# Kernel optimization log

Hardware: AMD Instinct MI355X
Metric: run time of the kernel (lower is better)

Reference implementation:

```python
import jax, jax.numpy as jnp
import numpy as np
import math

B, T, C, H = 4, 1024, 1024, 16
D = C // H  # head dim = 64

def setup_inputs() -> dict:
    key = jax.random.key(0)
    ks = jax.random.split(key, 10)
    s = 1.0 / math.sqrt(C)
    x = jax.random.normal(ks[0], (B, T, C), dtype=jnp.float32)
    pad = (jax.random.uniform(ks[1], (B, T)) < 0.2).astype(jnp.float32)
    # ensure first token of every row is unpadded so softmax rows are well-posed
    pad = pad.at[:, 0].set(0.0)
    Wq = jax.random.normal(ks[2], (C, C), dtype=jnp.float32) * s
    bq = jnp.zeros((C,), dtype=jnp.float32)
    Wk = jax.random.normal(ks[3], (C, C), dtype=jnp.float32) * s
    bk = jnp.zeros((C,), dtype=jnp.float32)
    Wv = jax.random.normal(ks[4], (C, C), dtype=jnp.float32) * s
    bv = jnp.zeros((C,), dtype=jnp.float32)
    Wp = jax.random.normal(ks[5], (C, C), dtype=jnp.float32) * s
    bp = jnp.zeros((C,), dtype=jnp.float32)
    return {"x": x, "x_padding_judge": pad, "Wq": Wq, "bq": bq,
            "Wk": Wk, "bk": bk, "Wv": Wv, "bv": bv, "Wp": Wp, "bp": bp}

def reference(x, x_padding_judge, Wq, bq, Wk, bk, Wv, bv, Wp, bp):
    # keep flag: 1.0 where token is real, 0.0 where padded
    keep = 1.0 - x_padding_judge                      # [B, T]
    mask = keep[:, :, None] * keep[:, None, :]        # [B, T, T] outer product
    # projections, split heads: [B, H, T, D]
    def heads(w, b):
        return (x @ w + b).reshape(B, T, H, D).transpose(0, 2, 1, 3)
    q, k, v = heads(Wq, bq), heads(Wk, bk), heads(Wv, bv)
    att = jnp.einsum('bhqd,bhkd->bhqk', q, k) * (1.0 / math.sqrt(D))
    # attn_pdrop=0 => att_full is all ones; masked_fill where mask == 0
    att = jnp.where(mask[:, None, :, :] == 0, -1e9, att)
    att = jax.nn.softmax(att, axis=-1)
    y = jnp.einsum('bhqk,bhkd->bhqd', att, v)         # [B, H, T, D]
    y = y.transpose(0, 2, 1, 3).reshape(B, T, C)
    return y @ Wp + bp
```

## Files before the change

kernel.cpp:

```cpp
#include <hip/hip_runtime.h>
#include <hip/hip_bf16.h>
#include <math.h>

#define Bb 4
#define Tt 1024
#define Cc 1024
#define Hh 16
#define Dd 64

typedef __attribute__((ext_vector_type(8))) _Float16 half8;
typedef __attribute__((ext_vector_type(4))) _Float16 half4;
typedef __attribute__((ext_vector_type(4))) float floatx4;


__global__ __launch_bounds__(256) void convert_fp16(const float* __restrict__ s,
                                                    _Float16* __restrict__ d)
{
    const int m16 = blockIdx.x;
    const int r   = threadIdx.x & 15;
    const int kc0 = threadIdx.x >> 4;
    const float* src = s + (size_t)(m16 * 16 + r) * 1024;
    _Float16*   dst = d + (size_t)m16 * 16384 + r * 8;
#pragma unroll
    for (int c8 = 0; c8 < 8; ++c8) {
        const int kc = kc0 + c8 * 16;
        float4 a = *(const float4*)(src + kc * 8);
        float4 b = *(const float4*)(src + kc * 8 + 4);
        half8 h;
        h[0] = (_Float16)a.x; h[1] = (_Float16)a.y; h[2] = (_Float16)a.z; h[3] = (_Float16)a.w;
        h[4] = (_Float16)b.x; h[5] = (_Float16)b.y; h[6] = (_Float16)b.z; h[7] = (_Float16)b.w;
        *(half8*)(dst + kc * 128) = h;
    }
}

struct WPrep { const float* W[4]; _Float16* out[4]; };

__global__ __launch_bounds__(256) void prep_weights(WPrep p)
{
    const int z = blockIdx.z;
    const float* __restrict__ W = p.W[z];
    _Float16* __restrict__ outp = p.out[z];
    __shared__ float tile[64][65];
    const int k0  = blockIdx.y * 64;
    const int n0  = blockIdx.x * 64;
    const int tr  = threadIdx.x >> 4;
    const int tc4 = (threadIdx.x & 15) * 4;

#pragma unroll
    for (int i = 0; i < 4; ++i) {
        const int kk = tr + i * 16;
        float4 v = *(const float4*)(W + (size_t)(k0 + kk) * 1024 + n0 + tc4);
        tile[kk][tc4 + 0] = v.x;
        tile[kk][tc4 + 1] = v.y;
        tile[kk][tc4 + 2] = v.z;
        tile[kk][tc4 + 3] = v.w;
    }
    __syncthreads();
#pragma unroll
    for (int i = 0; i < 4; ++i) {
        half4 h;
#pragma unroll
        for (int c = 0; c < 4; ++c) h[c] = (_Float16)tile[tc4 + c][tr + i * 16];
        _Float16* dst = outp + (size_t)((n0 >> 4) + i) * 16384
                        + ((k0 + tc4) >> 3) * 128 + tr * 8 + (tc4 & 7);
        *(half4*)dst = h;
    }
}

struct QkvP { const _Float16* Wt[3]; const float* bias[3];
              _Float16* qb; _Float16* kb; _Float16* vt; };

__global__ __launch_bounds__(256) void gemm_qkv(const _Float16* __restrict__ xh, QkvP p)
{
    const int z = blockIdx.z;
    const _Float16* __restrict__ Wt   = p.Wt[z];
    const float* __restrict__    bias = p.bias[z];

    const int tid  = threadIdx.x;
    const int lane = tid & 63;
    const int w    = tid >> 6;
    const int wr   = w >> 1, wc = w & 1;
    const int quad = lane >> 4;
    const int l15  = lane & 15;
    const int bm   = blockIdx.x * 128;
    const int bn   = blockIdx.y * 128;

    const _Float16* Ap[4];
    const _Float16* Bp[4];
#pragma unroll
    for (int i = 0; i < 4; ++i)
        Ap[i] = xh + (size_t)((bm >> 4) + wr * 4 + i) * 16384 + lane * 8;
#pragma unroll
    for (int j = 0; j < 4; ++j)
        Bp[j] = Wt + (size_t)((bn >> 4) + wc * 4 + j) * 16384 + lane * 8;

    floatx4 acc[4][4];
#pragma unroll
    for (int i = 0; i < 4; ++i)
#pragma unroll
        for (int j = 0; j < 4; ++j)
            acc[i][j] = (floatx4){0.f, 0.f, 0.f, 0.f};

    half8 a0[4], b0[4];
#pragma unroll
    for (int i = 0; i < 4; ++i) a0[i] = *(const half8*)(Ap[i]);
#pragma unroll
    for (int j = 0; j < 4; ++j) b0[j] = *(const half8*)(Bp[j]);

    for (int kt = 0; kt < 1024; kt += 64) {
        half8 a1[4], b1[4];
        const size_t o1 = (size_t)(kt + 32) * 16;
#pragma unroll
        for (int i = 0; i < 4; ++i) a1[i] = *(const half8*)(Ap[i] + o1);
#pragma unroll
        for (int j = 0; j < 4; ++j) b1[j] = *(const half8*)(Bp[j] + o1);
#pragma unroll
        for (int i = 0; i < 4; ++i)
#pragma unroll
            for (int j = 0; j < 4; ++j)
                acc[i][j] = __builtin_amdgcn_mfma_f32_16x16x32_f16(a0[i], b0[j], acc[i][j], 0, 0, 0);

        const size_t o2 = (kt + 64 < 1024) ? (size_t)(kt + 64) * 16 : 0;
#pragma unroll
        for (int i = 0; i < 4; ++i) a0[i] = *(const half8*)(Ap[i] + o2);
#pragma unroll
        for (int j = 0; j < 4; ++j) b0[j] = *(const half8*)(Bp[j] + o2);
#pragma unroll
        for (int i = 0; i < 4; ++i)
#pragma unroll
            for (int j = 0; j < 4; ++j)
                acc[i][j] = __builtin_amdgcn_mfma_f32_16x16x32_f16(a1[i], b1[j], acc[i][j], 0, 0, 0);
    }

    if (z == 2) {
#pragma unroll
        for (int j = 0; j < 4; ++j) {
            const int col = bn + wc * 64 + j * 16 + l15;
            const int h  = col >> 6;
            const float bj = bias[col];
#pragma unroll
            for (int i = 0; i < 4; ++i) {
                const int t0 = bm + wr * 64 + i * 16 + quad * 4;
                const int bh = (t0 >> 10) * 16 + h;
                const int tm = t0 & 1023;
                half4 pk;
#pragma unroll
                for (int r = 0; r < 4; ++r) pk[r] = (_Float16)(acc[i][j][r] + bj);
                *(half4*)(p.vt + (size_t)bh * 65536 + (size_t)j * 16384
                          + (tm >> 3) * 128 + l15 * 8 + (tm & 7)) = pk;
            }
        }
    } else {
        _Float16* outp = (z == 0) ? p.qb : p.kb;
#pragma unroll
        for (int j = 0; j < 4; ++j) {
            const int col = bn + wc * 64 + j * 16 + l15;
            const int h  = col >> 6;
            const int dd = col & 63;
            const float bj = bias[col];
            const int doff = (dd >> 3) * 128 + (dd & 7);
#pragma unroll
            for (int i = 0; i < 4; ++i) {
#pragma unroll
                for (int r = 0; r < 4; ++r) {
                    const int tg = bm + wr * 64 + i * 16 + quad * 4 + r;
                    const int bh = (tg >> 10) * 16 + h;
                    const int tm = tg & 1023;
                    outp[(size_t)bh * 65536 + (tm >> 4) * 1024 + doff + (tm & 15) * 8] =
                        (_Float16)(acc[i][j][r] + bj);
                }
            }
        }
    }
}

__global__ __launch_bounds__(256) void attn_mfma(
    const _Float16* __restrict__ qb, const _Float16* __restrict__ kb,
    const _Float16* __restrict__ vt, const float* __restrict__ padj,
    _Float16* __restrict__ yh)
{
    __shared__ __align__(16) _Float16 Ps[4][2048];

    const int tid  = threadIdx.x;
    const int lane = tid & 63;
    const int w    = tid >> 6;
    const int quad = lane >> 4;
    const int l15  = lane & 15;
    const int bh   = blockIdx.x;
    const int q0   = blockIdx.y * 128;
    const int b    = bh >> 4;
    const int h    = bh & 15;

    const _Float16* qf = qb + (size_t)bh * 65536;
    const _Float16* kf = kb + (size_t)bh * 65536;
    const _Float16* vf = vt + (size_t)bh * 65536;
    const float*    pk_row = padj + b * Tt;

    half8 bq[2][2];
#pragma unroll
    for (int ks = 0; ks < 2; ++ks)
#pragma unroll
        for (int nq = 0; nq < 2; ++nq)
            bq[ks][nq] = *(const half8*)(qf + (size_t)((q0 >> 4) + w * 2 + nq) * 1024
                                         + ks * 512 + lane * 8);
    float kq[2];
#pragma unroll
    for (int nq = 0; nq < 2; ++nq)
        kq[nq] = 1.0f - pk_row[q0 + w * 32 + nq * 16 + l15];

    floatx4 O[2][4];
    floatx4 l_acc[2];
#pragma unroll
    for (int mi = 0; mi < 2; ++mi) {
#pragma unroll
        for (int dj = 0; dj < 4; ++dj) O[mi][dj] = (floatx4){0.f, 0.f, 0.f, 0.f};
        l_acc[mi] = (floatx4){0.f, 0.f, 0.f, 0.f};
    }
    half8 ones;
#pragma unroll
    for (int j = 0; j < 8; ++j) ones[j] = (_Float16)1.0f;

    constexpr float SC = 0.18033688011112042f;

    for (int kt = 0; kt < Tt; kt += 64) {
        half8 ak[2][4], bv[2][4];
#pragma unroll
        for (int ks = 0; ks < 2; ++ks)
#pragma unroll
            for (int mk = 0; mk < 4; ++mk)
                ak[ks][mk] = *(const half8*)(kf + (size_t)((kt >> 4) + mk) * 1024
                                             + ks * 512 + lane * 8);
#pragma unroll
        for (int ks = 0; ks < 2; ++ks)
#pragma unroll
            for (int dj = 0; dj < 4; ++dj)
                bv[ks][dj] = *(const half8*)(vf + (size_t)dj * 16384 + (kt >> 3) * 128
                                             + ks * 512 + lane * 8);
        float4 kk4[4];
#pragma unroll
        for (int mk = 0; mk < 4; ++mk)
            kk4[mk] = *(const float4*)(pk_row + kt + mk * 16 + quad * 4);

        floatx4 ST[4][2];
#pragma unroll
        for (int mk = 0; mk < 4; ++mk)
#pragma unroll
            for (int nq = 0; nq < 2; ++nq)
                ST[mk][nq] = (floatx4){0.f, 0.f, 0.f, 0.f};
#pragma unroll
        for (int ks = 0; ks < 2; ++ks)
#pragma unroll
            for (int mk = 0; mk < 4; ++mk)
#pragma unroll
                for (int nq = 0; nq < 2; ++nq)
                    ST[mk][nq] = __builtin_amdgcn_mfma_f32_16x16x32_f16(
                        ak[ks][mk], bq[ks][nq], ST[mk][nq], 0, 0, 0);

#pragma unroll
        for (int mk = 0; mk < 4; ++mk) {
            const float kkr[4] = {1.0f - kk4[mk].x, 1.0f - kk4[mk].y,
                                  1.0f - kk4[mk].z, 1.0f - kk4[mk].w};
#pragma unroll
            for (int nq = 0; nq < 2; ++nq) {
                half4 pk;
#pragma unroll
                for (int r = 0; r < 4; ++r) {
                    const float e = __builtin_amdgcn_exp2f(ST[mk][nq][r] * SC);
                    const float pv = (kq[nq] == 0.0f) ? 1.0f : kkr[r] * e;
                    pk[r] = (_Float16)pv;
                }
                *(half4*)&Ps[w][((mk * 2 + (quad >> 1)) * 32 + nq * 16 + l15) * 8
                               + (quad & 1) * 4] = pk;
            }
        }

#pragma unroll
        for (int ks = 0; ks < 2; ++ks) {
            half8 ap[2];
#pragma unroll
            for (int mi = 0; mi < 2; ++mi)
                ap[mi] = *(const half8*)&Ps[w][((ks * 4 + quad) * 32 + mi * 16 + l15) * 8];
#pragma unroll
            for (int mi = 0; mi < 2; ++mi) {
#pragma unroll
                for (int dj = 0; dj < 4; ++dj)
                    O[mi][dj] = __builtin_amdgcn_mfma_f32_16x16x32_f16(
                        ap[mi], bv[ks][dj], O[mi][dj], 0, 0, 0);
                l_acc[mi] = __builtin_amdgcn_mfma_f32_16x16x32_f16(
                    ap[mi], ones, l_acc[mi], 0, 0, 0);
            }
        }
    }

#pragma unroll
    for (int mi = 0; mi < 2; ++mi) {
#pragma unroll
        for (int r = 0; r < 4; ++r) {
            const int rowl  = w * 32 + mi * 16 + quad * 4 + r;
            const int token = b * Tt + q0 + rowl;
            const float inv = 1.0f / l_acc[mi][r];
            const size_t tb = (size_t)(token >> 4) * 16384 + (token & 15) * 8;
#pragma unroll
            for (int dj = 0; dj < 4; ++dj) {
                const int col = h * 64 + dj * 16 + l15;
                yh[tb + (col >> 3) * 128 + (col & 7)] = (_Float16)(O[mi][dj][r] * inv);
            }
        }
    }
}

__global__ __launch_bounds__(256) void gemm_proj(const _Float16* __restrict__ Ay,
                                                 const _Float16* __restrict__ Bt,
                                                 const float* __restrict__ bias,
                                                 float* __restrict__ out)
{
    const int tid  = threadIdx.x;
    const int lane = tid & 63;
    const int w    = tid >> 6;
    const int quad = lane >> 4;
    const int l15  = lane & 15;
    const int bm   = blockIdx.x * 128;
    const int bn   = blockIdx.y * 64;

    const _Float16* Ap[2];
    const _Float16* Bp[4];
#pragma unroll
    for (int i = 0; i < 2; ++i)
        Ap[i] = Ay + (size_t)((bm >> 4) + w * 2 + i) * 16384 + lane * 8;
#pragma unroll
    for (int j = 0; j < 4; ++j)
        Bp[j] = Bt + (size_t)((bn >> 4) + j) * 16384 + lane * 8;

    floatx4 acc[2][4];
#pragma unroll
    for (int i = 0; i < 2; ++i)
#pragma unroll
        for (int j = 0; j < 4; ++j)
            acc[i][j] = (floatx4){0.f, 0.f, 0.f, 0.f};

    half8 a0[2], b0[4];
#pragma unroll
    for (int i = 0; i < 2; ++i) a0[i] = *(const half8*)(Ap[i]);
#pragma unroll
    for (int j = 0; j < 4; ++j) b0[j] = *(const half8*)(Bp[j]);

    for (int kt = 0; kt < 1024; kt += 64) {
        half8 a1[2], b1[4];
        const size_t o1 = (size_t)(kt + 32) * 16;
#pragma unroll
        for (int i = 0; i < 2; ++i) a1[i] = *(const half8*)(Ap[i] + o1);
#pragma unroll
        for (int j = 0; j < 4; ++j) b1[j] = *(const half8*)(Bp[j] + o1);
#pragma unroll
        for (int i = 0; i < 2; ++i)
#pragma unroll
            for (int j = 0; j < 4; ++j)
                acc[i][j] = __builtin_amdgcn_mfma_f32_16x16x32_f16(a0[i], b0[j], acc[i][j], 0, 0, 0);

        const size_t o2 = (kt + 64 < 1024) ? (size_t)(kt + 64) * 16 : 0;
#pragma unroll
        for (int i = 0; i < 2; ++i) a0[i] = *(const half8*)(Ap[i] + o2);
#pragma unroll
        for (int j = 0; j < 4; ++j) b0[j] = *(const half8*)(Bp[j] + o2);
#pragma unroll
        for (int i = 0; i < 2; ++i)
#pragma unroll
            for (int j = 0; j < 4; ++j)
                acc[i][j] = __builtin_amdgcn_mfma_f32_16x16x32_f16(a1[i], b1[j], acc[i][j], 0, 0, 0);
    }

#pragma unroll
    for (int j = 0; j < 4; ++j) {
        const int col = bn + j * 16 + l15;
        const float bj = bias[col];
#pragma unroll
        for (int i = 0; i < 2; ++i) {
            const int row = bm + w * 32 + i * 16 + quad * 4;
            float* o = out + (size_t)row * 1024 + col;
#pragma unroll
            for (int r = 0; r < 4; ++r)
                o[(size_t)r * 1024] = acc[i][j][r] + bj;
        }
    }
}

extern "C" void kernel_launch(void* const* d_in, const int* in_sizes, int n_in,
                              void* d_out, int out_size, void* d_ws, size_t ws_size,
                              hipStream_t stream)
{
    const float* x    = (const float*)d_in[0];
    const float* padj = (const float*)d_in[1];
    const float* Wq   = (const float*)d_in[2];
    const float* bq   = (const float*)d_in[3];
    const float* Wk   = (const float*)d_in[4];
    const float* bk   = (const float*)d_in[5];
    const float* Wv   = (const float*)d_in[6];
    const float* bv   = (const float*)d_in[7];
    const float* Wp   = (const float*)d_in[8];
    const float* bp   = (const float*)d_in[9];
    float* out = (float*)d_out;

    const size_t MB = 1024 * 1024;
    char* ws = (char*)d_ws;
    _Float16* xh  = (_Float16*)(ws);
    _Float16* Wt0 = (_Float16*)(ws +  8 * MB);
    _Float16* Wt1 = (_Float16*)(ws + 10 * MB);
    _Float16* Wt2 = (_Float16*)(ws + 12 * MB);
    _Float16* Wtp = (_Float16*)(ws + 14 * MB);
    _Float16* qb  = (_Float16*)(ws + 16 * MB);
    _Float16* kb  = (_Float16*)(ws + 24 * MB);
    _Float16* vtb = (_Float16*)(ws + 32 * MB);
    _Float16* yh  = (_Float16*)(ws + 40 * MB);

    convert_fp16<<<256, 256, 0, stream>>>(x, xh);

    WPrep wp;
    wp.W[0] = Wq; wp.W[1] = Wk; wp.W[2] = Wv; wp.W[3] = Wp;
    wp.out[0] = Wt0; wp.out[1] = Wt1; wp.out[2] = Wt2; wp.out[3] = Wtp;
    prep_weights<<<dim3(16, 16, 4), 256, 0, stream>>>(wp);

    QkvP qp;
    qp.Wt[0] = Wt0; qp.Wt[1] = Wt1; qp.Wt[2] = Wt2;
    qp.bias[0] = bq; qp.bias[1] = bk; qp.bias[2] = bv;
    qp.qb = qb; qp.kb = kb; qp.vt = vtb;
    gemm_qkv<<<dim3(32, 8, 3), 256, 0, stream>>>(xh, qp);

    attn_mfma<<<dim3(64, 8), 256, 0, stream>>>(qb, kb, vtb, padj, yh);

    gemm_proj<<<dim3(32, 16), 256, 0, stream>>>(yh, Wtp, bp, out);
}
```

Baseline: 188.6 us.

## Merge prep kernels, transpose Q/K GEMM for vector stores, widen attention to 8 waves

Folds the x conversion and weight transposition into one prep_all launch to save a kernel launch. For the Q and K projections it swaps the GEMM operands (weights as A, x as B), so each lane holds four consecutive head-dim values and writes them as one half4 instead of four scalar stores. The attention kernel moves to 512 threads with 16 query rows per wave instead of 32, which halves per-wave register state and raises wave count, but each wave now gets less reuse of the K and V fragments it loads.

```diff
diff --git a/kernel.cpp b/kernel.cpp
--- a/kernel.cpp
+++ b/kernel.cpp
@@ -13,36 +13,36 @@
 typedef __attribute__((ext_vector_type(4))) float floatx4;
 
 
-__global__ __launch_bounds__(256) void convert_fp16(const float* __restrict__ s,
-                                                    _Float16* __restrict__ d)
+struct PrepP { const float* x; _Float16* xh; const float* W[4]; _Float16* out[4]; };
+
+__global__ __launch_bounds__(256) void prep_all(PrepP p)
 {
-    const int m16 = blockIdx.x;
-    const int r   = threadIdx.x & 15;
-    const int kc0 = threadIdx.x >> 4;
-    const float* src = s + (size_t)(m16 * 16 + r) * 1024;
-    _Float16*   dst = d + (size_t)m16 * 16384 + r * 8;
-#pragma unroll
-    for (int c8 = 0; c8 < 8; ++c8) {
-        const int kc = kc0 + c8 * 16;
-        float4 a = *(const float4*)(src + kc * 8);
-        float4 b = *(const float4*)(src + kc * 8 + 4);
-        half8 h;
-        h[0] = (_Float16)a.x; h[1] = (_Float16)a.y; h[2] = (_Float16)a.z; h[3] = (_Float16)a.w;
-        h[4] = (_Float16)b.x; h[5] = (_Float16)b.y; h[6] = (_Float16)b.z; h[7] = (_Float16)b.w;
-        *(half8*)(dst + kc * 128) = h;
-    }
-}
-
-struct WPrep { const float* W[4]; _Float16* out[4]; };
-
-__global__ __launch_bounds__(256) void prep_weights(WPrep p)
-{
-    const int z = blockIdx.z;
+    if (blockIdx.x < 256) {
+        const int m16 = blockIdx.x;
+        const int r   = threadIdx.x & 15;
+        const int kc0 = threadIdx.x >> 4;
+        const float* src = p.x + (size_t)(m16 * 16 + r) * 1024;
+        _Float16*   dst = p.xh + (size_t)m16 * 16384 + r * 8;
+#pragma unroll
+        for (int c8 = 0; c8 < 8; ++c8) {
+            const int kc = kc0 + c8 * 16;
+            float4 a = *(const float4*)(src + kc * 8);
+            float4 b = *(const float4*)(src + kc * 8 + 4);
+            half8 h;
+            h[0] = (_Float16)a.x; h[1] = (_Float16)a.y; h[2] = (_Float16)a.z; h[3] = (_Float16)a.w;
+            h[4] = (_Float16)b.x; h[5] = (_Float16)b.y; h[6] = (_Float16)b.z; h[7] = (_Float16)b.w;
+            *(half8*)(dst + kc * 128) = h;
+        }
+        return;
+    }
+    const int bid2 = blockIdx.x - 256;
+    const int z    = bid2 >> 8;
+    const int rem  = bid2 & 255;
+    const int n0   = (rem & 15) * 64;
+    const int k0   = (rem >> 4) * 64;
     const float* __restrict__ W = p.W[z];
     _Float16* __restrict__ outp = p.out[z];
     __shared__ float tile[64][65];
-    const int k0  = blockIdx.y * 64;
-    const int n0  = blockIdx.x * 64;
     const int tr  = threadIdx.x >> 4;
     const int tc4 = (threadIdx.x & 15) * 4;
 
@@ -73,8 +73,7 @@
 __global__ __launch_bounds__(256) void gemm_qkv(const _Float16* __restrict__ xh, QkvP p)
 {
     const int z = blockIdx.z;
-    const _Float16* __restrict__ Wt   = p.Wt[z];
-    const float* __restrict__    bias = p.bias[z];
+    const float* __restrict__ bias = p.bias[z];
 
     const int tid  = threadIdx.x;
     const int lane = tid & 63;
@@ -82,17 +81,20 @@
     const int wr   = w >> 1, wc = w & 1;
     const int quad = lane >> 4;
     const int l15  = lane & 15;
-    const int bm   = blockIdx.x * 128;
-    const int bn   = blockIdx.y * 128;
+
+    const int mb = (z == 2) ? blockIdx.x * 128 : blockIdx.y * 128;
+    const int nb = (z == 2) ? blockIdx.y * 128 : blockIdx.x * 128;
+    const _Float16* __restrict__ Abase = (z == 2) ? xh : p.Wt[z];
+    const _Float16* __restrict__ Bbase = (z == 2) ? p.Wt[2] : xh;
 
     const _Float16* Ap[4];
     const _Float16* Bp[4];
 #pragma unroll
     for (int i = 0; i < 4; ++i)
-        Ap[i] = xh + (size_t)((bm >> 4) + wr * 4 + i) * 16384 + lane * 8;
+        Ap[i] = Abase + (size_t)((mb >> 4) + wr * 4 + i) * 16384 + lane * 8;
 #pragma unroll
     for (int j = 0; j < 4; ++j)
-        Bp[j] = Wt + (size_t)((bn >> 4) + wc * 4 + j) * 16384 + lane * 8;
+        Bp[j] = Bbase + (size_t)((nb >> 4) + wc * 4 + j) * 16384 + lane * 8;
 
     floatx4 acc[4][4];
 #pragma unroll
@@ -135,12 +137,12 @@
     if (z == 2) {
 #pragma unroll
         for (int j = 0; j < 4; ++j) {
-            const int col = bn + wc * 64 + j * 16 + l15;
+            const int col = nb + wc * 64 + j * 16 + l15;
             const int h  = col >> 6;
             const float bj = bias[col];
 #pragma unroll
             for (int i = 0; i < 4; ++i) {
-                const int t0 = bm + wr * 64 + i * 16 + quad * 4;
+                const int t0 = mb + wr * 64 + i * 16 + quad * 4;
                 const int bh = (t0 >> 10) * 16 + h;
                 const int tm = t0 & 1023;
                 half4 pk;
@@ -154,32 +156,34 @@
         _Float16* outp = (z == 0) ? p.qb : p.kb;
 #pragma unroll
         for (int j = 0; j < 4; ++j) {
-            const int col = bn + wc * 64 + j * 16 + l15;
-            const int h  = col >> 6;
-            const int dd = col & 63;
-            const float bj = bias[col];
-            const int doff = (dd >> 3) * 128 + (dd & 7);
+            const int token = nb + wc * 64 + j * 16 + l15;
+            const int bi = token >> 10;
+            const int tm = token & 1023;
+            const size_t tb = (size_t)(tm >> 4) * 1024 + (tm & 15) * 8;
 #pragma unroll
             for (int i = 0; i < 4; ++i) {
-#pragma unroll
-                for (int r = 0; r < 4; ++r) {
-                    const int tg = bm + wr * 64 + i * 16 + quad * 4 + r;
-                    const int bh = (tg >> 10) * 16 + h;
-                    const int tm = tg & 1023;
-                    outp[(size_t)bh * 65536 + (tm >> 4) * 1024 + doff + (tm & 15) * 8] =
-                        (_Float16)(acc[i][j][r] + bj);
-                }
+                const int colb = mb + wr * 64 + i * 16 + quad * 4;
+                const int h  = colb >> 6;
+                const int d  = colb & 63;
+                const float4 b4 = *(const float4*)(bias + colb);
+                half4 pk;
+                pk[0] = (_Float16)(acc[i][j][0] + b4.x);
+                pk[1] = (_Float16)(acc[i][j][1] + b4.y);
+                pk[2] = (_Float16)(acc[i][j][2] + b4.z);
+                pk[3] = (_Float16)(acc[i][j][3] + b4.w);
+                *(half4*)(outp + (size_t)(bi * 16 + h) * 65536 + tb
+                          + (d >> 3) * 128 + (d & 7)) = pk;
             }
         }
     }
 }
 
-__global__ __launch_bounds__(256) void attn_mfma(
+__global__ __launch_bounds__(512) void attn_mfma(
     const _Float16* __restrict__ qb, const _Float16* __restrict__ kb,
     const _Float16* __restrict__ vt, const float* __restrict__ padj,
     _Float16* __restrict__ yh)
 {
-    __shared__ __align__(16) _Float16 Ps[4][2048];
+    __shared__ __align__(16) _Float16 Ps[8][1024];
 
     const int tid  = threadIdx.x;
     const int lane = tid & 63;
@@ -196,26 +200,17 @@
     const _Float16* vf = vt + (size_t)bh * 65536;
     const float*    pk_row = padj + b * Tt;
 
-    half8 bq[2][2];
+    half8 bq[2];
 #pragma unroll
     for (int ks = 0; ks < 2; ++ks)
-#pragma unroll
-        for (int nq = 0; nq < 2; ++nq)
-            bq[ks][nq] = *(const half8*)(qf + (size_t)((q0 >> 4) + w * 2 + nq) * 1024
-                                         + ks * 512 + lane * 8);
-    float kq[2];
-#pragma unroll
-    for (int nq = 0; nq < 2; ++nq)
-        kq[nq] = 1.0f - pk_row[q0 + w * 32 + nq * 16 + l15];
-
-    floatx4 O[2][4];
-    floatx4 l_acc[2];
-#pragma unroll
-    for (int mi = 0; mi < 2; ++mi) {
-#pragma unroll
-        for (int dj = 0; dj < 4; ++dj) O[mi][dj] = (floatx4){0.f, 0.f, 0.f, 0.f};
-        l_acc[mi] = (floatx4){0.f, 0.f, 0.f, 0.f};
-    }
+        bq[ks] = *(const half8*)(qf + (size_t)((q0 >> 4) + w) * 1024 + ks * 512 + lane * 8);
+    const float kq = 1.0f - pk_row[q0 + w * 16 + l15];
+
+    floatx4 O[4];
+    floatx4 l_acc = (floatx4){0.f, 0.f, 0.f, 0.f};
+#pragma unroll
+    for (int dj = 0; dj < 4; ++dj) O[dj] = (floatx4){0.f, 0.f, 0.f, 0.f};
+
     half8 ones;
 #pragma unroll
     for (int j = 0; j < 8; ++j) ones[j] = (_Float16)1.0f;
@@ -241,70 +236,49 @@
         for (int mk = 0; mk < 4; ++mk)
             kk4[mk] = *(const float4*)(pk_row + kt + mk * 16 + quad * 4);
 
-        floatx4 ST[4][2];
-#pragma unroll
-        for (int mk = 0; mk < 4; ++mk)
-#pragma unroll
-            for (int nq = 0; nq < 2; ++nq)
-                ST[mk][nq] = (floatx4){0.f, 0.f, 0.f, 0.f};
+        floatx4 ST[4];
+#pragma unroll
+        for (int mk = 0; mk < 4; ++mk) ST[mk] = (floatx4){0.f, 0.f, 0.f, 0.f};
 #pragma unroll
         for (int ks = 0; ks < 2; ++ks)
 #pragma unroll
             for (int mk = 0; mk < 4; ++mk)
-#pragma unroll
-                for (int nq = 0; nq < 2; ++nq)
-                    ST[mk][nq] = __builtin_amdgcn_mfma_f32_16x16x32_f16(
-                        ak[ks][mk], bq[ks][nq], ST[mk][nq], 0, 0, 0);
+                ST[mk] = __builtin_amdgcn_mfma_f32_16x16x32_f16(ak[ks][mk], bq[ks], ST[mk], 0, 0, 0);
 
 #pragma unroll
         for (int mk = 0; mk < 4; ++mk) {
             const float kkr[4] = {1.0f - kk4[mk].x, 1.0f - kk4[mk].y,
                                   1.0f - kk4[mk].z, 1.0f - kk4[mk].w};
-#pragma unroll
-            for (int nq = 0; nq < 2; ++nq) {
-                half4 pk;
-#pragma unroll
-                for (int r = 0; r < 4; ++r) {
-                    const float e = __builtin_amdgcn_exp2f(ST[mk][nq][r] * SC);
-                    const float pv = (kq[nq] == 0.0f) ? 1.0f : kkr[r] * e;
-                    pk[r] = (_Float16)pv;
-                }
-                *(half4*)&Ps[w][((mk * 2 + (quad >> 1)) * 32 + nq * 16 + l15) * 8
-                               + (quad & 1) * 4] = pk;
+            half4 pk;
+#pragma unroll
+            for (int r = 0; r < 4; ++r) {
+                const float e = __builtin_amdgcn_exp2f(ST[mk][r] * SC);
+                const float pv = (kq == 0.0f) ? 1.0f : kkr[r] * e;
+                pk[r] = (_Float16)pv;
             }
+            *(half4*)&Ps[w][((mk * 2 + (quad >> 1)) * 16 + l15) * 8 + (quad & 1) * 4] = pk;
         }
 
 #pragma unroll
         for (int ks = 0; ks < 2; ++ks) {
-            half8 ap[2];
-#pragma unroll
-            for (int mi = 0; mi < 2; ++mi)
-                ap[mi] = *(const half8*)&Ps[w][((ks * 4 + quad) * 32 + mi * 16 + l15) * 8];
-#pragma unroll
-            for (int mi = 0; mi < 2; ++mi) {
-#pragma unroll
-                for (int dj = 0; dj < 4; ++dj)
-                    O[mi][dj] = __builtin_amdgcn_mfma_f32_16x16x32_f16(
-                        ap[mi], bv[ks][dj], O[mi][dj], 0, 0, 0);
-                l_acc[mi] = __builtin_amdgcn_mfma_f32_16x16x32_f16(
-                    ap[mi], ones, l_acc[mi], 0, 0, 0);
-            }
-        }
-    }
-
-#pragma unroll
-    for (int mi = 0; mi < 2; ++mi) {
-#pragma unroll
-        for (int r = 0; r < 4; ++r) {
-            const int rowl  = w * 32 + mi * 16 + quad * 4 + r;
-            const int token = b * Tt + q0 + rowl;
-            const float inv = 1.0f / l_acc[mi][r];
-            const size_t tb = (size_t)(token >> 4) * 16384 + (token & 15) * 8;
-#pragma unroll
-            for (int dj = 0; dj < 4; ++dj) {
-                const int col = h * 64 + dj * 16 + l15;
-                yh[tb + (col >> 3) * 128 + (col & 7)] = (_Float16)(O[mi][dj][r] * inv);
-            }
+            half8 ap = *(const half8*)&Ps[w][((ks * 4 + quad) * 16 + l15) * 8];
+#pragma unroll
+            for (int dj = 0; dj < 4; ++dj)
+                O[dj] = __builtin_amdgcn_mfma_f32_16x16x32_f16(ap, bv[ks][dj], O[dj], 0, 0, 0);
+            l_acc = __builtin_amdgcn_mfma_f32_16x16x32_f16(ap, ones, l_acc, 0, 0, 0);
+        }
+    }
+
+#pragma unroll
+    for (int r = 0; r < 4; ++r) {
+        const int rowl  = w * 16 + quad * 4 + r;
+        const int token = b * Tt + q0 + rowl;
+        const float inv = 1.0f / l_acc[r];
+        const size_t tb = (size_t)(token >> 4) * 16384 + (token & 15) * 8;
+#pragma unroll
+        for (int dj = 0; dj < 4; ++dj) {
+            const int col = h * 64 + dj * 16 + l15;
+            yh[tb + (col >> 3) * 128 + (col & 7)] = (_Float16)(O[dj][r] * inv);
         }
     }
 }
@@ -412,12 +386,11 @@
     _Float16* vtb = (_Float16*)(ws + 32 * MB);
     _Float16* yh  = (_Float16*)(ws + 40 * MB);
 
-    convert_fp16<<<256, 256, 0, stream>>>(x, xh);
-
-    WPrep wp;
-    wp.W[0] = Wq; wp.W[1] = Wk; wp.W[2] = Wv; wp.W[3] = Wp;
-    wp.out[0] = Wt0; wp.out[1] = Wt1; wp.out[2] = Wt2; wp.out[3] = Wtp;
-    prep_weights<<<dim3(16, 16, 4), 256, 0, stream>>>(wp);
+    PrepP pp;
+    pp.x = x; pp.xh = xh;
+    pp.W[0] = Wq; pp.W[1] = Wk; pp.W[2] = Wv; pp.W[3] = Wp;
+    pp.out[0] = Wt0; pp.out[1] = Wt1; pp.out[2] = Wt2; pp.out[3] = Wtp;
+    prep_all<<<1280, 256, 0, stream>>>(pp);
 
     QkvP qp;
     qp.Wt[0] = Wt0; qp.Wt[1] = Wt1; qp.Wt[2] = Wt2;
@@ -425,7 +398,7 @@
     qp.qb = qb; qp.kb = kb; qp.vt = vtb;
     gemm_qkv<<<dim3(32, 8, 3), 256, 0, stream>>>(xh, qp);
 
-    attn_mfma<<<dim3(64, 8), 256, 0, stream>>>(qb, kb, vtb, padj, yh);
+    attn_mfma<<<dim3(64, 8), 512, 0, stream>>>(qb, kb, vtb, padj, yh);
 
     gemm_proj<<<dim3(32, 16), 256, 0, stream>>>(yh, Wtp, bp, out);
 }
```

Result: slower. 205.8 us (+9.1%).
